# Kernel optimization log

Measured on AMD Instinct MI355X. Metric: run time of the kernel, lower is better.

## Reference

```python
import jax, jax.numpy as jnp
import numpy as np

NUM_SHEET = 16; MAX_W = 128; MAX_H = 128; MAX_P = 25; HIDDEN = 1024
CNN_DIM = 4 * NUM_SHEET * (MAX_W // 4) * (MAX_H // 4)
IN_DIM = CNN_DIM + 3 * MAX_P
ACT_DIM = 2 * NUM_SHEET * MAX_P


def setup_inputs():
    key = jax.random.key(0)
    ks = jax.random.split(key, 8)
    r = jax.random.randint(ks[0], (NUM_SHEET, MAX_W, MAX_H), 0, 20)
    stocks = jnp.where(r > 0, -1, 0).astype(jnp.int32)
    prod_sizes = jax.random.randint(ks[1], (MAX_P, 2), 1, 16).astype(jnp.int32)
    prod_qty = jax.random.randint(ks[2], (MAX_P,), 0, 10).astype(jnp.int32)
    def rnd(k, shape, scale):
        return jax.random.normal(k, shape, jnp.float32) * scale
    return {
        'stocks': stocks, 'prod_sizes': prod_sizes, 'prod_qty': prod_qty,
        'conv1_w': rnd(ks[3], (2, 1, 3, 3), 0.3), 'conv1_b': jnp.zeros((2,), jnp.float32),
        'conv2_w': rnd(ks[4], (4, 2, 3, 3), 0.2), 'conv2_b': jnp.zeros((4,), jnp.float32),
        'fc1_w': rnd(ks[5], (IN_DIM, HIDDEN), 0.004), 'fc1_b': jnp.zeros((HIDDEN,), jnp.float32),
        'fc2_w': rnd(ks[6], (HIDDEN, ACT_DIM), 0.03), 'fc2_b': jnp.zeros((ACT_DIM,), jnp.float32),
    }


def _valid_actions(stocks, sizes, qty):
    # Integral-image replacement for the O(sheet*product*W*H*w*h) nested-loop scan.
    filled = (stocks != -1).astype(jnp.int32)  # [S, W, H]
    ii = jnp.cumsum(jnp.cumsum(filled, axis=1), axis=2)
    ii = jnp.pad(ii, ((0, 0), (1, 0), (1, 0)))  # summed-area table [S, W+1, H+1]
    i = jnp.arange(MAX_W)[:, None]
    j = jnp.arange(MAX_H)[None, :]

    def fits(sat, wh):
        w, h = wh[0], wh[1]
        i2 = jnp.minimum(i + w, MAX_W)
        j2 = jnp.minimum(j + h, MAX_H)
        win = sat[i2, j2] - sat[i, j2] - sat[i2, j] + sat[i, j]  # filled count per window
        ok = (i <= MAX_W - w) & (j <= MAX_H - h)
        return jnp.any(ok & (win == 0))

    v0 = jax.vmap(lambda sat: jax.vmap(lambda wh: fits(sat, wh))(sizes))(ii)          # [S, P]
    v1 = jax.vmap(lambda sat: jax.vmap(lambda wh: fits(sat, wh[::-1]))(sizes))(ii)    # rotated
    v1 = v1 & ~v0  # original breaks out of the orientation loop once m=0 is valid
    have = (qty > 0)[None, :]
    valid = jnp.stack([v0 & have, v1 & have], axis=-1)  # [S, P, 2] -> index (s*P+p)*2+m
    return valid.reshape(-1)


def reference(stocks, prod_sizes, prod_qty, conv1_w, conv1_b, conv2_w, conv2_b, fc1_w, fc1_b, fc2_w, fc2_b):
    # preprocess: 1.0 where empty (-1); batch the per-sheet conv loop over the sheet axis
    x = (stocks == -1).astype(jnp.float32)[:, None]  # [S, 1, W, H]
    dn = ('NCHW', 'OIHW', 'NCHW')
    x = jax.nn.relu(jax.lax.conv_general_dilated(x, conv1_w, (2, 2), ((1, 1), (1, 1)), dimension_numbers=dn) + conv1_b[None, :, None, None])
    x = jax.nn.relu(jax.lax.conv_general_dilated(x, conv2_w, (2, 2), ((1, 1), (1, 1)), dimension_numbers=dn) + conv2_b[None, :, None, None])
    cnn_out = x.reshape(1, -1)  # per-sheet flatten then concat == sheet-major reshape
    pf = jnp.concatenate([prod_sizes.astype(jnp.float32), prod_qty.astype(jnp.float32)[:, None]], axis=1).reshape(1, -1)  # [1, 3P]
    combined = jnp.concatenate([cnn_out, pf], axis=1)  # [1, IN_DIM]
    h = jax.nn.relu(combined @ fc1_w + fc1_b)
    logits = h @ fc2_w + fc2_b  # [1, ACT_DIM]
    valid = _valid_actions(stocks, prod_sizes, prod_qty)
    logits = jnp.where(valid[None, :], logits, jnp.float32(-1e9))
    return jax.nn.softmax(logits, axis=1)
```

## Files before the change

kernel.cpp:

```cpp
#include <hip/hip_runtime.h>
#include <hip/hip_bf16.h>
#include <cstdint>

#define NSHEET 16
#define MAXW 128
#define MAXH 128
#define MAXP 25
#define HIDDEN 1024
#define CNN_DIM 65536
#define IN_DIM 65611
#define ACT_DIM 800
#define CHUNK 128
#define NCHUNK 513
#define NVALID 800
#define FC2_BLOCKS 32

#define OFF_COMB 0
#define OFF_SAT  262656
#define OFF_P1   786944
#define OFF_H    2888192
#define OFF_FITS 2892288
#define OFF_P2   2895488

__global__ __launch_bounds__(256) void k1_prep(
        const int* __restrict__ stocks, const int* __restrict__ psz,
        const int* __restrict__ pq,
        const float* __restrict__ c1w, const float* __restrict__ c1b,
        const float* __restrict__ c2w, const float* __restrict__ c2b,
        float* __restrict__ comb, unsigned short* __restrict__ satg)
{
    __shared__ __align__(16) unsigned char smem[49664];
    const int tid = threadIdx.x;
    if (blockIdx.x < NSHEET) {
        const int s = blockIdx.x;
        unsigned char* xs = smem;
        float* o1 = (float*)(smem + 16384);
        float* wb = (float*)(smem + 16384 + 32768);
        const int* st = stocks + s * 16384;
        for (int k = 0; k < 64; ++k) {
            int idx = tid + k * 256;
            xs[idx] = (st[idx] == -1) ? 1 : 0;
        }
        if (tid < 96) {
            float v;
            if (tid < 18)      v = c1w[tid];
            else if (tid < 20) v = c1b[tid - 18];
            else if (tid < 92) v = c2w[tid - 20];
            else               v = c2b[tid - 92];
            wb[tid] = v;
        }
        __syncthreads();
        for (int k = 0; k < 32; ++k) {
            int idx = tid + k * 256;
            int oc = idx >> 12;
            int r = idx & 4095;
            int oy = r >> 6, ox = r & 63;
            float acc = wb[18 + oc];
            #pragma unroll
            for (int ky = 0; ky < 3; ++ky) {
                int iy = 2 * oy - 1 + ky;
                if (iy < 0 || iy > 127) continue;
                #pragma unroll
                for (int kx = 0; kx < 3; ++kx) {
                    int ix = 2 * ox - 1 + kx;
                    if (ix < 0 || ix > 127) continue;
                    acc += (float)xs[iy * 128 + ix] * wb[oc * 9 + ky * 3 + kx];
                }
            }
            o1[idx] = fmaxf(acc, 0.f);
        }
        __syncthreads();
        for (int k = 0; k < 16; ++k) {
            int idx = tid + k * 256;
            int oc = idx >> 10;
            int r = idx & 1023;
            int oy = r >> 5, ox = r & 31;
            float acc = wb[92 + oc];
            #pragma unroll
            for (int ic = 0; ic < 2; ++ic)
            #pragma unroll
            for (int ky = 0; ky < 3; ++ky) {
                int iy = 2 * oy - 1 + ky;
                if (iy < 0 || iy > 63) continue;
                #pragma unroll
                for (int kx = 0; kx < 3; ++kx) {
                    int ix = 2 * ox - 1 + kx;
                    if (ix < 0 || ix > 63) continue;
                    acc += o1[ic * 4096 + iy * 64 + ix] *
                           wb[20 + ((oc * 2 + ic) * 9 + ky * 3 + kx)];
                }
            }
            comb[s * 4096 + idx] = fmaxf(acc, 0.f);
        }
        if (s == 0 && tid < 3 * MAXP) {
            int p = tid / 3, r = tid - p * 3;
            comb[CNN_DIM + tid] = (float)(r < 2 ? psz[p * 2 + r] : pq[p]);
        }
    } else {
        const int s = blockIdx.x - NSHEET;
        unsigned short* sat = (unsigned short*)smem;
        const int* st = stocks + s * 16384;
        for (int k = 0; k < 64; ++k) {
            int idx = tid + k * 256;
            sat[(idx >> 7) * 132 + (idx & 127)] = (st[idx] != -1) ? 1 : 0;
        }
        __syncthreads();
        if (tid < 128) {
            int run = 0;
            for (int c = 0; c < 128; ++c) {
                run += sat[tid * 132 + c];
                sat[tid * 132 + c] = (unsigned short)run;
            }
        }
        __syncthreads();
        if (tid < 128) {
            int run = 0;
            for (int r = 0; r < 128; ++r) {
                run += sat[r * 132 + tid];
                sat[r * 132 + tid] = (unsigned short)run;
            }
        }
        __syncthreads();
        for (int k = 0; k < 64; ++k) {
            int idx = tid + k * 256;
            satg[s * 16384 + idx] = sat[(idx >> 7) * 132 + (idx & 127)];
        }
    }
}

__global__ __launch_bounds__(256) void k2_fc1_valid(
        const float* __restrict__ comb, const float* __restrict__ fc1w,
        const unsigned short* __restrict__ satg, const int* __restrict__ psz,
        float* __restrict__ part1, int* __restrict__ fits)
{
    const int tid = threadIdx.x;
    if (blockIdx.x < NCHUNK) {
        const int b = blockIdx.x;
        const int base = b * CHUNK;
        const int nr = min(CHUNK, IN_DIM - base);
        __shared__ float cval[CHUNK];
        __shared__ int   cidx[CHUNK];
        __shared__ int   wcnt[2];
        float v = 0.f; bool nz = false; int pre = 0;
        if (tid < CHUNK) {
            if (tid < nr) v = comb[base + tid];
            nz = (v != 0.f);
            unsigned long long m = __ballot(nz);
            int lane = tid & 63;
            pre = __popcll(m & ((1ull << lane) - 1ull));
            if (lane == 0) wcnt[tid >> 6] = __popcll(m);
        }
        __syncthreads();
        const int w0c = wcnt[0];
        const int total = w0c + wcnt[1];
        if (nz) {
            int pos = ((tid >> 6) ? w0c : 0) + pre;
            cval[pos] = v;
            cidx[pos] = base + tid;
        }
        __syncthreads();
        float4 acc = {0.f, 0.f, 0.f, 0.f};
        const float4* W4 = (const float4*)fc1w;
        int i = 0;
        for (; i + 4 <= total; i += 4) {
            int r0 = cidx[i], r1 = cidx[i + 1], r2 = cidx[i + 2], r3 = cidx[i + 3];
            float4 a0 = W4[r0 * 256 + tid];
            float4 a1 = W4[r1 * 256 + tid];
            float4 a2 = W4[r2 * 256 + tid];
            float4 a3 = W4[r3 * 256 + tid];
            float c0 = cval[i], c1 = cval[i + 1], c2 = cval[i + 2], c3 = cval[i + 3];
            acc.x += c0 * a0.x; acc.y += c0 * a0.y; acc.z += c0 * a0.z; acc.w += c0 * a0.w;
            acc.x += c1 * a1.x; acc.y += c1 * a1.y; acc.z += c1 * a1.z; acc.w += c1 * a1.w;
            acc.x += c2 * a2.x; acc.y += c2 * a2.y; acc.z += c2 * a2.z; acc.w += c2 * a2.w;
            acc.x += c3 * a3.x; acc.y += c3 * a3.y; acc.z += c3 * a3.z; acc.w += c3 * a3.w;
        }
        for (; i < total; ++i) {
            float cv = cval[i];
            float4 w = W4[cidx[i] * 256 + tid];
            acc.x += cv * w.x; acc.y += cv * w.y;
            acc.z += cv * w.z; acc.w += cv * w.w;
        }
        ((float4*)part1)[b * 256 + tid] = acc;
    } else {
        const int vb = blockIdx.x - NCHUNK;
        const int s = vb / 50, pm = vb - s * 50;
        const int p = pm >> 1, m = pm & 1;
        const int w = psz[p * 2 + m];
        const int h = psz[p * 2 + 1 - m];
        const unsigned short* S = satg + s * 16384;
        const int imax = MAXW - w, jmax = MAXH - h;
        __shared__ int found;
        if (tid == 0) found = 0;
        __syncthreads();
        int f = 0;
        for (int pos = tid; pos < 16384; pos += 256) {
            int i = pos >> 7, j = pos & 127;
            if (i <= imax && j <= jmax) {
                int i2 = i + w - 1, j2 = j + h - 1;
                int sum = (int)S[i2 * 128 + j2]
                        - (i ? (int)S[(i - 1) * 128 + j2] : 0)
                        - (j ? (int)S[i2 * 128 + (j - 1)] : 0)
                        + ((i && j) ? (int)S[(i - 1) * 128 + (j - 1)] : 0);
                if (sum == 0) f = 1;
            }
        }
        if (f) atomicOr(&found, 1);
        __syncthreads();
        if (tid == 0) fits[s * 50 + pm] = found;
    }
}

__global__ __launch_bounds__(256) void k3a_hred(
        const float* __restrict__ part1, const float* __restrict__ fc1b,
        float* __restrict__ h)
{
    const int j0 = blockIdx.x * 16;
    const int lane16 = threadIdx.x & 15;
    const int r = threadIdx.x >> 4;
    float s = 0.f;
    for (int c = r; c < NCHUNK; c += 16)
        s += part1[c * 1024 + j0 + lane16];
    __shared__ float red[16][17];
    red[r][lane16] = s;
    __syncthreads();
    if (threadIdx.x < 16) {
        float t = fc1b[j0 + threadIdx.x];
        #pragma unroll
        for (int k = 0; k < 16; ++k) t += red[k][threadIdx.x];
        h[j0 + threadIdx.x] = fmaxf(t, 0.f);
    }
}

__global__ __launch_bounds__(256) void k3b_fc2part(
        const float* __restrict__ h, const float* __restrict__ fc2w,
        float* __restrict__ part2)
{
    const int b = blockIdx.x;
    const int tid = threadIdx.x;
    const int k0 = b * 32;
    __shared__ float hl[32];
    if (tid < 32) hl[tid] = h[k0 + tid];
    __syncthreads();
    const int a4 = tid * 4;
    if (a4 < ACT_DIM) {
        float4 acc = {0.f, 0.f, 0.f, 0.f};
        #pragma unroll 4
        for (int k = 0; k < 32; ++k) {
            float hv = hl[k];
            if (hv == 0.f) continue;
            const float4 w = *(const float4*)(fc2w + (size_t)(k0 + k) * ACT_DIM + a4);
            acc.x += hv * w.x; acc.y += hv * w.y;
            acc.z += hv * w.z; acc.w += hv * w.w;
        }
        *(float4*)(part2 + b * ACT_DIM + a4) = acc;
    }
}

__global__ __launch_bounds__(256) void k4_final(
        const float* __restrict__ part2, const float* __restrict__ fc2b,
        const int* __restrict__ fits, const int* __restrict__ pq,
        float* __restrict__ out)
{
    const int tid = threadIdx.x;
    __shared__ float lg[ACT_DIM];
    __shared__ float red[8];
    __shared__ float gval[2];
    for (int a = tid; a < ACT_DIM; a += 256) {
        float v = fc2b[a];
        #pragma unroll
        for (int c = 0; c < FC2_BLOCKS; ++c) v += part2[c * ACT_DIM + a];
        int m = a & 1, t2 = a >> 1;
        int p = t2 % 25, s = t2 / 25;
        int v0 = fits[s * 50 + p * 2];
        int v1 = fits[s * 50 + p * 2 + 1];
        bool valid = (m == 0 ? (v0 != 0) : (v1 != 0 && v0 == 0)) && (pq[p] > 0);
        lg[a] = valid ? v : -1e9f;
    }
    __syncthreads();
    float lm = -3e38f;
    for (int a = tid; a < ACT_DIM; a += 256) lm = fmaxf(lm, lg[a]);
    for (int off = 32; off >= 1; off >>= 1) lm = fmaxf(lm, __shfl_down(lm, off));
    if ((tid & 63) == 0) red[tid >> 6] = lm;
    __syncthreads();
    if (tid == 0) {
        float m = red[0];
        for (int w = 1; w < 4; ++w) m = fmaxf(m, red[w]);
        gval[0] = m;
    }
    __syncthreads();
    const float gmax = gval[0];
    float ls = 0.f;
    for (int a = tid; a < ACT_DIM; a += 256) {
        float e = expf(lg[a] - gmax);
        lg[a] = e;
        ls += e;
    }
    for (int off = 32; off >= 1; off >>= 1) ls += __shfl_down(ls, off);
    if ((tid & 63) == 0) red[tid >> 6] = ls;
    __syncthreads();
    if (tid == 0) gval[1] = red[0] + red[1] + red[2] + red[3];
    __syncthreads();
    const float inv = 1.f / gval[1];
    for (int a = tid; a < ACT_DIM; a += 256) out[a] = lg[a] * inv;
}

extern "C" void kernel_launch(void* const* d_in, const int* in_sizes, int n_in,
                              void* d_out, int out_size, void* d_ws, size_t ws_size,
                              hipStream_t stream) {
    const int*   stocks = (const int*)d_in[0];
    const int*   psz    = (const int*)d_in[1];
    const int*   pq     = (const int*)d_in[2];
    const float* c1w    = (const float*)d_in[3];
    const float* c1b    = (const float*)d_in[4];
    const float* c2w    = (const float*)d_in[5];
    const float* c2b    = (const float*)d_in[6];
    const float* fc1w   = (const float*)d_in[7];
    const float* fc1b   = (const float*)d_in[8];
    const float* fc2w   = (const float*)d_in[9];
    const float* fc2b   = (const float*)d_in[10];
    float* out = (float*)d_out;
    char*  ws  = (char*)d_ws;

    float*          comb  = (float*)(ws + OFF_COMB);
    unsigned short* satg  = (unsigned short*)(ws + OFF_SAT);
    float*          part1 = (float*)(ws + OFF_P1);
    float*          hbuf  = (float*)(ws + OFF_H);
    int*            fitsp = (int*)(ws + OFF_FITS);
    float*          part2 = (float*)(ws + OFF_P2);

    hipLaunchKernelGGL(k1_prep, dim3(2 * NSHEET), dim3(256), 0, stream,
                       stocks, psz, pq, c1w, c1b, c2w, c2b, comb, satg);
    hipLaunchKernelGGL(k2_fc1_valid, dim3(NCHUNK + NVALID), dim3(256), 0, stream,
                       comb, fc1w, satg, psz, part1, fitsp);
    hipLaunchKernelGGL(k3a_hred, dim3(64), dim3(256), 0, stream,
                       part1, fc1b, hbuf);
    hipLaunchKernelGGL(k3b_fc2part, dim3(FC2_BLOCKS), dim3(256), 0, stream,
                       hbuf, fc2w, part2);
    hipLaunchKernelGGL(k4_final, dim3(1), dim3(256), 0, stream,
                       part2, fc2b, fitsp, pq, out);
}
```

Baseline: 405.2 us.

## Halve fc1 chunk size, prefetch gathered weight rows, widen partial reduction

Fc1 chunks shrink from 128 to 64 input rows, which doubles the number of blocks so more sparse row gathers run in parallel. The nonzero compaction now needs only a single wavefront ballot. The gather loop is padded to multiples of 8 and software-prefetches the next 8 weight rows while accumulating the current ones, which hides memory latency. The reduction kernel uses 1024 threads to sum twice as many partials, at the cost of a larger partial buffer and extra reduction traffic.

```diff
diff --git a/kernel.cpp b/kernel.cpp
--- a/kernel.cpp
+++ b/kernel.cpp
@@ -10,17 +10,17 @@
 #define CNN_DIM 65536
 #define IN_DIM 65611
 #define ACT_DIM 800
-#define CHUNK 128
-#define NCHUNK 513
+#define CHUNK 64
+#define NCHUNK 1026
 #define NVALID 800
 #define FC2_BLOCKS 32
 
 #define OFF_COMB 0
 #define OFF_SAT  262656
 #define OFF_P1   786944
-#define OFF_H    2888192
-#define OFF_FITS 2892288
-#define OFF_P2   2895488
+#define OFF_H    4989440
+#define OFF_FITS 4993536
+#define OFF_P2   4996736
 
 __global__ __launch_bounds__(256) void k1_prep(
         const int* __restrict__ stocks, const int* __restrict__ psz,
@@ -138,47 +138,47 @@
         const int b = blockIdx.x;
         const int base = b * CHUNK;
         const int nr = min(CHUNK, IN_DIM - base);
-        __shared__ float cval[CHUNK];
-        __shared__ int   cidx[CHUNK];
-        __shared__ int   wcnt[2];
-        float v = 0.f; bool nz = false; int pre = 0;
-        if (tid < CHUNK) {
-            if (tid < nr) v = comb[base + tid];
-            nz = (v != 0.f);
+        __shared__ float cval[CHUNK + 8];
+        __shared__ int   cidx[CHUNK + 8];
+        __shared__ int   tot;
+        if (tid < 64) {
+            float v = (tid < nr) ? comb[base + tid] : 0.f;
+            bool nz = (v != 0.f);
             unsigned long long m = __ballot(nz);
-            int lane = tid & 63;
-            pre = __popcll(m & ((1ull << lane) - 1ull));
-            if (lane == 0) wcnt[tid >> 6] = __popcll(m);
-        }
-        __syncthreads();
-        const int w0c = wcnt[0];
-        const int total = w0c + wcnt[1];
-        if (nz) {
-            int pos = ((tid >> 6) ? w0c : 0) + pre;
-            cval[pos] = v;
-            cidx[pos] = base + tid;
-        }
-        __syncthreads();
+            int pre = __popcll(m & ((1ull << tid) - 1ull));
+            if (nz) { cval[pre] = v; cidx[pre] = base + tid; }
+            if (tid == 0) {
+                int t = __popcll(m);
+                int tp = (t + 7) & ~7;
+                for (int u = t; u < tp; ++u) { cval[u] = 0.f; cidx[u] = base; }
+                tot = tp;
+            }
+        }
+        __syncthreads();
+        const int totp = tot;
         float4 acc = {0.f, 0.f, 0.f, 0.f};
         const float4* W4 = (const float4*)fc1w;
-        int i = 0;
-        for (; i + 4 <= total; i += 4) {
-            int r0 = cidx[i], r1 = cidx[i + 1], r2 = cidx[i + 2], r3 = cidx[i + 3];
-            float4 a0 = W4[r0 * 256 + tid];
-            float4 a1 = W4[r1 * 256 + tid];
-            float4 a2 = W4[r2 * 256 + tid];
-            float4 a3 = W4[r3 * 256 + tid];
-            float c0 = cval[i], c1 = cval[i + 1], c2 = cval[i + 2], c3 = cval[i + 3];
-            acc.x += c0 * a0.x; acc.y += c0 * a0.y; acc.z += c0 * a0.z; acc.w += c0 * a0.w;
-            acc.x += c1 * a1.x; acc.y += c1 * a1.y; acc.z += c1 * a1.z; acc.w += c1 * a1.w;
-            acc.x += c2 * a2.x; acc.y += c2 * a2.y; acc.z += c2 * a2.z; acc.w += c2 * a2.w;
-            acc.x += c3 * a3.x; acc.y += c3 * a3.y; acc.z += c3 * a3.z; acc.w += c3 * a3.w;
-        }
-        for (; i < total; ++i) {
-            float cv = cval[i];
-            float4 w = W4[cidx[i] * 256 + tid];
-            acc.x += cv * w.x; acc.y += cv * w.y;
-            acc.z += cv * w.z; acc.w += cv * w.w;
+        if (totp > 0) {
+            float4 g[8]; float cv[8];
+            #pragma unroll
+            for (int u = 0; u < 8; ++u) {
+                g[u] = W4[cidx[u] * 256 + tid];
+                cv[u] = cval[u];
+            }
+            for (int i = 0; i < totp; i += 8) {
+                const bool more = (i + 8) < totp;
+                #pragma unroll
+                for (int u = 0; u < 8; ++u) {
+                    float4 w = g[u]; float c = cv[u];
+                    if (more) {
+                        int nx = i + 8 + u;
+                        g[u] = W4[cidx[nx] * 256 + tid];
+                        cv[u] = cval[nx];
+                    }
+                    acc.x += c * w.x; acc.y += c * w.y;
+                    acc.z += c * w.z; acc.w += c * w.w;
+                }
+            }
         }
         ((float4*)part1)[b * 256 + tid] = acc;
     } else {
@@ -210,23 +210,23 @@
     }
 }
 
-__global__ __launch_bounds__(256) void k3a_hred(
+__global__ __launch_bounds__(1024) void k3a_hred(
         const float* __restrict__ part1, const float* __restrict__ fc1b,
         float* __restrict__ h)
 {
     const int j0 = blockIdx.x * 16;
-    const int lane16 = threadIdx.x & 15;
-    const int r = threadIdx.x >> 4;
+    const int l = threadIdx.x & 15;
+    const int g = threadIdx.x >> 4;
     float s = 0.f;
-    for (int c = r; c < NCHUNK; c += 16)
-        s += part1[c * 1024 + j0 + lane16];
-    __shared__ float red[16][17];
-    red[r][lane16] = s;
+    for (int c = g; c < NCHUNK; c += 64)
+        s += part1[c * 1024 + j0 + l];
+    __shared__ float red[64][17];
+    red[g][l] = s;
     __syncthreads();
     if (threadIdx.x < 16) {
         float t = fc1b[j0 + threadIdx.x];
-        #pragma unroll
-        for (int k = 0; k < 16; ++k) t += red[k][threadIdx.x];
+        #pragma unroll 8
+        for (int k = 0; k < 64; ++k) t += red[k][threadIdx.x];
         h[j0 + threadIdx.x] = fmaxf(t, 0.f);
     }
 }
@@ -332,7 +332,7 @@
                        stocks, psz, pq, c1w, c1b, c2w, c2b, comb, satg);
     hipLaunchKernelGGL(k2_fc1_valid, dim3(NCHUNK + NVALID), dim3(256), 0, stream,
                        comb, fc1w, satg, psz, part1, fitsp);
-    hipLaunchKernelGGL(k3a_hred, dim3(64), dim3(256), 0, stream,
+    hipLaunchKernelGGL(k3a_hred, dim3(64), dim3(1024), 0, stream,
                        part1, fc1b, hbuf);
     hipLaunchKernelGGL(k3b_fc2part, dim3(FC2_BLOCKS), dim3(256), 0, stream,
                        hbuf, fc2w, part2);
```

Measured after the change: 407.5 us. No clear change (+0.6%).
